# Kernel optimization log

Hardware: AMD Instinct MI355X
Metric: run time of the kernel (lower is better)

## Reference

```python
import jax, jax.numpy as jnp
import numpy as np

CLIP = 50.0
EPS = 1e-8


def _attn_jacobian_agg(q, k, v, scale):
    """Aggregate attention Jacobian dO/dq summed over queries, plus attention outputs.

    q: (B, Q, d); k, v: (B, S, d).
    Per-query Jacobian: J_q = scale * sum_j p_j v_j (k_j - kbar)^T, kbar = sum_i p_i k_i.
    Returns (agg_jac: (B, d, d), outputs: (B, Q, d)).
    """
    scores = jnp.einsum('bqd,bsd->bqs', q, k) * scale
    p = jax.nn.softmax(scores, axis=-1)
    out = jnp.einsum('bqs,bsd->bqd', p, v)           # attention outputs O
    kbar = jnp.einsum('bqs,bsd->bqd', p, k)          # expected key per query
    # sum_j p_j v_j k_j^T  -> (B, Q, d, d)
    pvk = jnp.einsum('bqs,bsd,bse->bqde', p, v, k)
    jac = scale * (pvk - out[..., :, None] * kbar[..., None, :])
    return jac.sum(axis=1), out


def setup_inputs() -> dict:
    key = jax.random.key(0)
    ks = jax.random.split(key, 5)
    B, Q, S, M, D = 256, 16, 512, 8, 128
    return {
        'queries': jax.random.normal(ks[0], (B, Q, D), dtype=jnp.float32),
        'keys':    jax.random.normal(ks[1], (B, S, D), dtype=jnp.float32),
        'values':  jax.random.normal(ks[2], (B, S, D), dtype=jnp.float32),
        'k_cg':    jax.random.normal(ks[3], (B, M, D), dtype=jnp.float32),
        'v_cg':    jax.random.normal(ks[4], (B, M, D), dtype=jnp.float32),
    }


def reference(queries, keys, values, k_cg, v_cg):
    B, Q, d = queries.shape
    scale = d ** -0.5

    dense_jac, dense_out = _attn_jacobian_agg(queries, keys, values, scale)
    cg_jac, cg_out = _attn_jacobian_agg(queries, k_cg, v_cg, scale)

    # jacobian_clip_value = 50.0 (config default)
    dense_jac = jnp.clip(dense_jac, -CLIP, CLIP)
    cg_jac = jnp.clip(cg_jac, -CLIP, CLIP)

    df = dense_jac.reshape(B, -1)
    cf = cg_jac.reshape(B, -1)
    dn = jnp.linalg.norm(df, axis=-1)
    cn = jnp.linalg.norm(cf, axis=-1)
    cosine_sim = (df * cf).sum(axis=-1) / (dn * cn + EPS)
    force_direction_loss = 1.0 - cosine_sim

    # consistency: per-query output MSE, averaged over queries, scaled by 1/d_head
    out_diff = dense_out - cg_out
    per_query_mse = (out_diff ** 2).sum(axis=-1)          # (B, Q)
    consistency_loss = per_query_mse.sum(axis=-1) / Q / d  # (B,)

    # v4 loss: L = w_dir * L_force_cos + w_cons * L_consistency (defaults 1.0, 1.0)
    total = 1.0 * force_direction_loss + 1.0 * consistency_loss
    return total.mean()  # reduction='mean'
```

## Files before the change

kernel.cpp:

```cpp
#include <hip/hip_runtime.h>
#include <math.h>


namespace {
constexpr int Bn = 256, Qn = 16, Sn = 512, Mn = 8, Dn = 128;
constexpr int NT = 512;
constexpr float SCALE = 0.08838834764831845f;
constexpr float CLIPV = 50.0f;

constexpr int W_OFF_F = 1048576;
constexpr int PCG_OFF_B = 4718592;
constexpr int WC_OFF_F = 1196032;
constexpr int PART_OFF_F = 1198080;

typedef __attribute__((ext_vector_type(8))) short bf16x8;
typedef __attribute__((ext_vector_type(4))) float f32x4;
#define MFMA16(a, b, c) __builtin_amdgcn_mfma_f32_16x16x32_bf16((a), (b), (c), 0, 0, 0)

__device__ inline unsigned int pack2t(float a, float b) {
  return __builtin_amdgcn_perm(__builtin_bit_cast(unsigned int, b),
                               __builtin_bit_cast(unsigned int, a), 0x07060302u);
}
__device__ inline unsigned short f2bf(float x) {
  unsigned int u = __builtin_bit_cast(unsigned int, x);
  u += 0x7fffu + ((u >> 16) & 1u);
  return (unsigned short)(u >> 16);
}
__device__ inline float bf2f(unsigned short h) {
  unsigned int u = ((unsigned int)h) << 16;
  return __builtin_bit_cast(float, u);
}
union Frag {
  bf16x8 v;
  unsigned int u[4];
  unsigned short h[8];
};

constexpr int A_QS = 0, A_PB = 4352, A_RDM = 20992, A_RDS = 21504,
              A_CGS = 22016, A_CGP = 22528, A_LDSZ = 22784;

__global__ __launch_bounds__(NT) void scores_kernel(
    const float* __restrict__ Qg, const float* __restrict__ Kg,
    const float* __restrict__ Kcg, float* __restrict__ ws) {
  __shared__ __align__(16) char L[A_LDSZ];
  const int b = blockIdx.x, t = threadIdx.x;
  const int lane = t & 63, wv = t >> 6, quad = lane >> 4, l16 = lane & 15;
  const float* Qb = Qg + (size_t)b * Qn * Dn;
  const float* Kb = Kg + (size_t)b * Sn * Dn;
  const float* Kc = Kcg + (size_t)b * Mn * Dn;

  if (t == 0)
    *(float4*)(ws + PART_OFF_F + b * 4) = make_float4(0.f, 0.f, 0.f, 0.f);

  {
    int row = t >> 5, c4 = t & 31;
    float4 qv = ((const float4*)Qb)[t];
    unsigned int p0 = pack2t(qv.x * SCALE, qv.y * SCALE);
    unsigned int p1 = pack2t(qv.z * SCALE, qv.w * SCALE);
    *(unsigned long long*)(L + A_QS + row * 272 + c4 * 8) =
        (unsigned long long)p0 | ((unsigned long long)p1 << 32);
  }
  __syncthreads();

  bf16x8 aq[4];
#pragma unroll
  for (int kk = 0; kk < 4; ++kk)
    aq[kk] = *(const bf16x8*)(L + A_QS + l16 * 272 + kk * 64 + quad * 16);
  f32x4 acc[4];
#pragma unroll
  for (int j = 0; j < 4; ++j) {
    const float* kp = Kb + (size_t)(64 * wv + 16 * j + l16) * Dn + quad * 8;
    f32x4 a = {0.f, 0.f, 0.f, 0.f};
#pragma unroll
    for (int kk = 0; kk < 4; ++kk) {
      float4 lo = *(const float4*)(kp + kk * 32);
      float4 hi = *(const float4*)(kp + kk * 32 + 4);
      Frag f;
      f.u[0] = pack2t(lo.x, lo.y);
      f.u[1] = pack2t(lo.z, lo.w);
      f.u[2] = pack2t(hi.x, hi.y);
      f.u[3] = pack2t(hi.z, hi.w);
      a = MFMA16(aq[kk], f.v, a);
    }
    acc[j] = a;
  }
  {
    float pm[4];
#pragma unroll
    for (int r = 0; r < 4; ++r)
      pm[r] = fmaxf(fmaxf(acc[0][r], acc[1][r]), fmaxf(acc[2][r], acc[3][r]));
#pragma unroll
    for (int o = 1; o < 16; o <<= 1)
#pragma unroll
      for (int r = 0; r < 4; ++r) pm[r] = fmaxf(pm[r], __shfl_xor(pm[r], o));
    if (l16 == 0)
#pragma unroll
      for (int r = 0; r < 4; ++r) *(float*)(L + A_RDM + (quad * 4 + r) * 32 + wv * 4) = pm[r];
  }
  __syncthreads();
  float gm[4];
#pragma unroll
  for (int r = 0; r < 4; ++r) {
    const float* p = (const float*)(L + A_RDM + (quad * 4 + r) * 32);
    float m = p[0];
#pragma unroll
    for (int w = 1; w < 8; ++w) m = fmaxf(m, p[w]);
    gm[r] = m;
  }
  float e[4][4];
  {
    float ps[4] = {0.f, 0.f, 0.f, 0.f};
#pragma unroll
    for (int j = 0; j < 4; ++j)
#pragma unroll
      for (int r = 0; r < 4; ++r) {
        e[j][r] = __expf(acc[j][r] - gm[r]);
        ps[r] += e[j][r];
      }
#pragma unroll
    for (int o = 1; o < 16; o <<= 1)
#pragma unroll
      for (int r = 0; r < 4; ++r) ps[r] += __shfl_xor(ps[r], o);
    if (l16 == 0)
#pragma unroll
      for (int r = 0; r < 4; ++r) *(float*)(L + A_RDS + (quad * 4 + r) * 32 + wv * 4) = ps[r];
  }
  __syncthreads();
  float inv[4];
#pragma unroll
  for (int r = 0; r < 4; ++r) {
    const float* p = (const float*)(L + A_RDS + (quad * 4 + r) * 32);
    float s = 0.f;
#pragma unroll
    for (int w = 0; w < 8; ++w) s += p[w];
    inv[r] = 1.f / s;
  }
#pragma unroll
  for (int j = 0; j < 4; ++j)
#pragma unroll
    for (int r = 0; r < 4; ++r)
      *(unsigned short*)(L + A_PB + (quad * 4 + r) * 1040 + (64 * wv + 16 * j + l16) * 2) =
          f2bf(e[j][r] * inv[r]);
  __syncthreads();
  {
    float wsum = 0.f;
#pragma unroll
    for (int q = 0; q < Qn; ++q)
      wsum += bf2f(*(const unsigned short*)(L + A_PB + q * 1040 + t * 2));
    ws[W_OFF_F + b * 512 + t] = wsum;
  }
#pragma unroll
  for (int i = 0; i < 2; ++i) {
    int idx = t + i * 512, q = idx >> 6, c = idx & 63;
    *(uint4*)((char*)ws + (size_t)b * 16384 + q * 1024 + c * 16) =
        *(const uint4*)(L + A_PB + q * 1040 + c * 16);
  }
  if (wv == 0) {
    const float* kp = Kc + (size_t)(l16 & 7) * Dn + quad * 8;
    f32x4 a = {0.f, 0.f, 0.f, 0.f};
#pragma unroll
    for (int kk = 0; kk < 4; ++kk) {
      float4 lo = *(const float4*)(kp + kk * 32);
      float4 hi = *(const float4*)(kp + kk * 32 + 4);
      Frag f;
      f.u[0] = pack2t(lo.x, lo.y);
      f.u[1] = pack2t(lo.z, lo.w);
      f.u[2] = pack2t(hi.x, hi.y);
      f.u[3] = pack2t(hi.z, hi.w);
      a = MFMA16(aq[kk], f.v, a);
    }
    if (l16 < 8)
#pragma unroll
      for (int r = 0; r < 4; ++r)
        *(float*)(L + A_CGS + (quad * 4 + r) * 32 + l16 * 4) = a[r];
  }
  __syncthreads();
  if (t < 16) {
    float xs[8];
    float m = -1e30f;
#pragma unroll
    for (int s = 0; s < 8; ++s) {
      xs[s] = *(const float*)(L + A_CGS + t * 32 + s * 4);
      m = fmaxf(m, xs[s]);
    }
    float ssum = 0.f;
#pragma unroll
    for (int s = 0; s < 8; ++s) {
      xs[s] = __expf(xs[s] - m);
      ssum += xs[s];
    }
    float iv = 1.f / ssum;
    uint4 pk = make_uint4(pack2t(xs[0] * iv, xs[1] * iv), pack2t(xs[2] * iv, xs[3] * iv),
                          pack2t(xs[4] * iv, xs[5] * iv), pack2t(xs[6] * iv, xs[7] * iv));
    *(uint4*)(L + A_CGP + t * 16) = pk;
    *(uint4*)((char*)ws + PCG_OFF_B + b * 256 + t * 16) = pk;
  }
  __syncthreads();
  if (t < 8) {
    float s = 0.f;
#pragma unroll
    for (int q = 0; q < Qn; ++q)
      s += bf2f(*(const unsigned short*)(L + A_CGP + q * 16 + t * 2));
    ws[WC_OFF_F + b * 8 + t] = s;
  }
}

constexpr int B_PB = 0, B_WOFF = 16640, B_KT = 18688, B_VT = 37120, B_VTW = 46336,
              B_PCG = 55552, B_WC = 56832, B_RED = 56864, B_LDSZ = 56992;

__global__ __launch_bounds__(NT, 4) void jac_kernel(
    const float* __restrict__ Kg, const float* __restrict__ Vg,
    const float* __restrict__ Kcg, const float* __restrict__ Vcg,
    float* __restrict__ ws) {
  __shared__ __align__(16) char L[B_LDSZ];
  const int g = blockIdx.x;
  const int h = (g >> 3) & 1;
  const int b = (g & 7) | ((g >> 4) << 3);
  const int t = threadIdx.x, lane = t & 63, wv = t >> 6;
  const int quad = lane >> 4, l16 = lane & 15;

  const float* Kb = Kg + (size_t)b * Sn * Dn;
  const float* Vb = Vg + (size_t)b * Sn * Dn;
  const float* Kc = Kcg + (size_t)b * Mn * Dn;
  const float* Vc = Vcg + (size_t)b * Mn * Dn;

  const int dK = t & 127, gK = t >> 7;
  const int dV = t & 63, gV = t >> 6;
  float kpf[2][8], vpf[8];

  auto load_tiles = [&](int st) {
#pragma unroll
    for (int o = 0; o < 2; ++o) {
      int s0 = st * 64 + (gK + 4 * o) * 8;
#pragma unroll
      for (int i = 0; i < 8; ++i) kpf[o][i] = Kb[(size_t)(s0 + i) * Dn + dK];
    }
    int s1 = st * 64 + gV * 8;
#pragma unroll
    for (int i = 0; i < 8; ++i) vpf[i] = Vb[(size_t)(s1 + i) * Dn + h * 64 + dV];
  };
  auto store_tiles = [&](int st) {
#pragma unroll
    for (int o = 0; o < 2; ++o) {
      unsigned int u0 = pack2t(kpf[o][0], kpf[o][1]), u1 = pack2t(kpf[o][2], kpf[o][3]);
      unsigned int u2 = pack2t(kpf[o][4], kpf[o][5]), u3 = pack2t(kpf[o][6], kpf[o][7]);
      *(uint4*)(L + B_KT + dK * 144 + (gK + 4 * o) * 16) = make_uint4(u0, u1, u2, u3);
    }
    int s1 = st * 64 + gV * 8;
    float w8[8];
#pragma unroll
    for (int i = 0; i < 8; ++i) w8[i] = *(const float*)(L + B_WOFF + (s1 + i) * 4);
    *(uint4*)(L + B_VT + dV * 144 + gV * 16) =
        make_uint4(pack2t(vpf[0], vpf[1]), pack2t(vpf[2], vpf[3]),
                   pack2t(vpf[4], vpf[5]), pack2t(vpf[6], vpf[7]));
    *(uint4*)(L + B_VTW + dV * 144 + gV * 16) =
        make_uint4(pack2t(w8[0] * vpf[0], w8[1] * vpf[1]), pack2t(w8[2] * vpf[2], w8[3] * vpf[3]),
                   pack2t(w8[4] * vpf[4], w8[5] * vpf[5]), pack2t(w8[6] * vpf[6], w8[7] * vpf[7]));
  };

#pragma unroll
  for (int i = 0; i < 2; ++i) {
    int idx = t + i * 512, q = idx >> 6, c = idx & 63;
    *(uint4*)(L + B_PB + q * 1040 + c * 16) =
        *(const uint4*)((const char*)ws + (size_t)b * 16384 + q * 1024 + c * 16);
  }
  *(float*)(L + B_WOFF + t * 4) = ws[W_OFF_F + b * 512 + t];
  if (t < 16) {
    uint4 pv = *(const uint4*)((const char*)ws + PCG_OFF_B + b * 256 + t * 16);
    *(uint4*)(L + B_PCG + t * 80) = pv;
    *(uint4*)(L + B_PCG + t * 80 + 16) = make_uint4(0, 0, 0, 0);
    *(uint4*)(L + B_PCG + t * 80 + 32) = make_uint4(0, 0, 0, 0);
    *(uint4*)(L + B_PCG + t * 80 + 48) = make_uint4(0, 0, 0, 0);
  }
  if (t < 8) *(float*)(L + B_WC + t * 4) = ws[WC_OFF_F + b * 8 + t];
  load_tiles(0);
  __syncthreads();

  const int rp = wv & 1, ch = wv >> 1;
  f32x4 C00 = {0.f,0.f,0.f,0.f}, C01 = {0.f,0.f,0.f,0.f};
  f32x4 C10 = {0.f,0.f,0.f,0.f}, C11 = {0.f,0.f,0.f,0.f};
  f32x4 outacc = {0.f,0.f,0.f,0.f}, kbacc = {0.f,0.f,0.f,0.f};

  auto ckstep = [&](int colByte, f32x4& c00, f32x4& c01, f32x4& c10, f32x4& c11) {
    bf16x8 A0 = *(const bf16x8*)(L + B_VTW + (rp * 32 + l16) * 144 + colByte + quad * 16);
    bf16x8 A1 = *(const bf16x8*)(L + B_VTW + (rp * 32 + 16 + l16) * 144 + colByte + quad * 16);
    bf16x8 B0 = *(const bf16x8*)(L + B_KT + (ch * 32 + l16) * 144 + colByte + quad * 16);
    bf16x8 B1 = *(const bf16x8*)(L + B_KT + (ch * 32 + 16 + l16) * 144 + colByte + quad * 16);
    c00 = MFMA16(A0, B0, c00);
    c01 = MFMA16(A0, B1, c01);
    c10 = MFMA16(A1, B0, c10);
    c11 = MFMA16(A1, B1, c11);
  };

  for (int st = 0; st < 8; ++st) {
    if (st) __syncthreads();
    store_tiles(st);
    __syncthreads();
    if (st < 7) load_tiles(st + 1);
#pragma unroll
    for (int z = 0; z < 2; ++z) {
      int colByte = z * 64;
      bf16x8 pA = *(const bf16x8*)(L + B_PB + l16 * 1040 + st * 128 + z * 64 + quad * 16);
      bf16x8 bK = *(const bf16x8*)(L + B_KT + (wv * 16 + l16) * 144 + colByte + quad * 16);
      kbacc = MFMA16(pA, bK, kbacc);
      if (wv < 4) {
        bf16x8 bV = *(const bf16x8*)(L + B_VT + (wv * 16 + l16) * 144 + colByte + quad * 16);
        outacc = MFMA16(pA, bV, outacc);
      }
      ckstep(colByte, C00, C01, C10, C11);
    }
  }
  __syncthreads();

  if (wv < 4) {
#pragma unroll
    for (int r = 0; r < 4; ++r)
      *(unsigned short*)(L + B_VTW + (wv * 16 + l16) * 144 + (quad * 4 + r) * 2) = f2bf(-outacc[r]);
  }
#pragma unroll
  for (int r = 0; r < 4; ++r)
    *(unsigned short*)(L + B_KT + (wv * 16 + l16) * 144 + (quad * 4 + r) * 2) = f2bf(kbacc[r]);
  if (t < 256) {
    *(uint4*)(L + B_KT + (t >> 1) * 144 + 32 + (t & 1) * 16) = make_uint4(0, 0, 0, 0);
  } else if (t < 384) {
    int i = t - 256;
    *(uint4*)(L + B_VTW + (i >> 1) * 144 + 32 + (i & 1) * 16) = make_uint4(0, 0, 0, 0);
  }
  __syncthreads();
  ckstep(0, C00, C01, C10, C11);
#pragma unroll
  for (int r = 0; r < 4; ++r) {
    C00[r] = fminf(fmaxf(SCALE * C00[r], -CLIPV), CLIPV);
    C01[r] = fminf(fmaxf(SCALE * C01[r], -CLIPV), CLIPV);
    C10[r] = fminf(fmaxf(SCALE * C10[r], -CLIPV), CLIPV);
    C11[r] = fminf(fmaxf(SCALE * C11[r], -CLIPV), CLIPV);
  }
  __syncthreads();

  if (t < 128) {
    float kv[8];
#pragma unroll
    for (int i = 0; i < 8; ++i) kv[i] = Kc[(size_t)i * Dn + t];
    *(uint4*)(L + B_KT + t * 144) = make_uint4(pack2t(kv[0], kv[1]), pack2t(kv[2], kv[3]),
                                               pack2t(kv[4], kv[5]), pack2t(kv[6], kv[7]));
    *(uint4*)(L + B_KT + t * 144 + 16) = make_uint4(0, 0, 0, 0);
    *(uint4*)(L + B_KT + t * 144 + 32) = make_uint4(0, 0, 0, 0);
    *(uint4*)(L + B_KT + t * 144 + 48) = make_uint4(0, 0, 0, 0);
  } else if (t < 192) {
    int d = t - 128;
    float v2[8];
#pragma unroll
    for (int i = 0; i < 8; ++i) v2[i] = Vc[(size_t)i * Dn + h * 64 + d];
    *(uint4*)(L + B_VT + d * 144) = make_uint4(pack2t(v2[0], v2[1]), pack2t(v2[2], v2[3]),
                                               pack2t(v2[4], v2[5]), pack2t(v2[6], v2[7]));
    *(uint4*)(L + B_VT + d * 144 + 16) = make_uint4(0, 0, 0, 0);
    *(uint4*)(L + B_VT + d * 144 + 32) = make_uint4(0, 0, 0, 0);
    *(uint4*)(L + B_VT + d * 144 + 48) = make_uint4(0, 0, 0, 0);
  } else if (t < 256) {
    int d = t - 192;
    float v2[8], wc[8];
#pragma unroll
    for (int i = 0; i < 8; ++i) {
      v2[i] = Vc[(size_t)i * Dn + h * 64 + d];
      wc[i] = *(const float*)(L + B_WC + i * 4);
    }
    *(uint4*)(L + B_VTW + d * 144) =
        make_uint4(pack2t(wc[0] * v2[0], wc[1] * v2[1]), pack2t(wc[2] * v2[2], wc[3] * v2[3]),
                   pack2t(wc[4] * v2[4], wc[5] * v2[5]), pack2t(wc[6] * v2[6], wc[7] * v2[7]));
    *(uint4*)(L + B_VTW + d * 144 + 16) = make_uint4(0, 0, 0, 0);
    *(uint4*)(L + B_VTW + d * 144 + 32) = make_uint4(0, 0, 0, 0);
    *(uint4*)(L + B_VTW + d * 144 + 48) = make_uint4(0, 0, 0, 0);
  }
  __syncthreads();
  f32x4 outc = {0.f,0.f,0.f,0.f}, kbc = {0.f,0.f,0.f,0.f};
  f32x4 D00 = {0.f,0.f,0.f,0.f}, D01 = {0.f,0.f,0.f,0.f};
  f32x4 D10 = {0.f,0.f,0.f,0.f}, D11 = {0.f,0.f,0.f,0.f};
  {
    bf16x8 pA = *(const bf16x8*)(L + B_PCG + l16 * 80 + quad * 16);
    bf16x8 bK = *(const bf16x8*)(L + B_KT + (wv * 16 + l16) * 144 + quad * 16);
    kbc = MFMA16(pA, bK, kbc);
    if (wv < 4) {
      bf16x8 bV = *(const bf16x8*)(L + B_VT + (wv * 16 + l16) * 144 + quad * 16);
      outc = MFMA16(pA, bV, outc);
    }
    ckstep(0, D00, D01, D10, D11);
  }
  __syncthreads();
  if (wv < 4) {
#pragma unroll
    for (int r = 0; r < 4; ++r)
      *(unsigned short*)(L + B_VTW + (wv * 16 + l16) * 144 + (quad * 4 + r) * 2) = f2bf(-outc[r]);
  }
#pragma unroll
  for (int r = 0; r < 4; ++r)
    *(unsigned short*)(L + B_KT + (wv * 16 + l16) * 144 + (quad * 4 + r) * 2) = f2bf(kbc[r]);
  __syncthreads();
  ckstep(0, D00, D01, D10, D11);
#pragma unroll
  for (int r = 0; r < 4; ++r) {
    D00[r] = fminf(fmaxf(SCALE * D00[r], -CLIPV), CLIPV);
    D01[r] = fminf(fmaxf(SCALE * D01[r], -CLIPV), CLIPV);
    D10[r] = fminf(fmaxf(SCALE * D10[r], -CLIPV), CLIPV);
    D11[r] = fminf(fmaxf(SCALE * D11[r], -CLIPV), CLIPV);
  }

  float dot = 0.f, nd2 = 0.f, nc2 = 0.f, cons = 0.f;
#pragma unroll
  for (int r = 0; r < 4; ++r) {
    dot += C00[r] * D00[r] + C01[r] * D01[r] + C10[r] * D10[r] + C11[r] * D11[r];
    nd2 += C00[r] * C00[r] + C01[r] * C01[r] + C10[r] * C10[r] + C11[r] * C11[r];
    nc2 += D00[r] * D00[r] + D01[r] * D01[r] + D10[r] * D10[r] + D11[r] * D11[r];
  }
  if (wv < 4) {
#pragma unroll
    for (int r = 0; r < 4; ++r) {
      float df = outacc[r] - outc[r];
      cons += df * df;
    }
  }
#pragma unroll
  for (int o = 32; o; o >>= 1) {
    dot += __shfl_xor(dot, o);
    nd2 += __shfl_xor(nd2, o);
    nc2 += __shfl_xor(nc2, o);
    cons += __shfl_xor(cons, o);
  }
  if (lane == 0) {
    float* red = (float*)(L + B_RED);
    red[wv * 4 + 0] = dot;
    red[wv * 4 + 1] = nd2;
    red[wv * 4 + 2] = nc2;
    red[wv * 4 + 3] = cons;
  }
  __syncthreads();
  if (t == 0) {
    const float* red = (const float*)(L + B_RED);
    float d_ = 0.f, n1 = 0.f, n2 = 0.f, cs = 0.f;
#pragma unroll
    for (int w = 0; w < 8; ++w) {
      d_ += red[w * 4 + 0];
      n1 += red[w * 4 + 1];
      n2 += red[w * 4 + 2];
      cs += red[w * 4 + 3];
    }
    atomicAdd(ws + PART_OFF_F + b * 4 + 0, d_);
    atomicAdd(ws + PART_OFF_F + b * 4 + 1, n1);
    atomicAdd(ws + PART_OFF_F + b * 4 + 2, n2);
    atomicAdd(ws + PART_OFF_F + b * 4 + 3, cs);
  }
}

__global__ void finalize_kernel(const float* __restrict__ ws, float* __restrict__ out) {
  __shared__ float sr[256];
  int i = threadIdx.x;
  const float* p = ws + PART_OFF_F + i * 4;
  float cosv = p[0] / (sqrtf(p[1]) * sqrtf(p[2]) + 1e-8f);
  sr[i] = (1.0f - cosv) + p[3] * (1.0f / (float)(Qn * Dn));
  __syncthreads();
  for (int off = 128; off; off >>= 1) {
    if (i < off) sr[i] += sr[i + off];
    __syncthreads();
  }
  if (i == 0) out[0] = sr[0] * (1.0f / (float)Bn);
}
}

extern "C" void kernel_launch(void* const* d_in, const int* in_sizes, int n_in,
                              void* d_out, int out_size, void* d_ws, size_t ws_size,
                              hipStream_t stream) {
  const float* q = (const float*)d_in[0];
  const float* k = (const float*)d_in[1];
  const float* v = (const float*)d_in[2];
  const float* kc = (const float*)d_in[3];
  const float* vc = (const float*)d_in[4];
  float* out = (float*)d_out;
  float* ws = (float*)d_ws;
  scores_kernel<<<Bn, NT, 0, stream>>>(q, k, kc, ws);
  jac_kernel<<<2 * Bn, NT, 0, stream>>>(k, v, kc, vc, ws);
  finalize_kernel<<<1, 256, 0, stream>>>(ws, out);
}
```

Measured before the change: 171.7 us.

## Split jacobian kernel into four quadrant blocks per batch with staggered tile order

The jacobian kernel now launches four blocks per batch instead of two. Each block computes a 64x64 quadrant of the d×d Jacobian, with K restricted to its half of the columns. The LDS footprint is roughly halved by reading the probability fragments directly from global memory instead of staging them, and launch bounds raise the occupancy target to 8 blocks. A per-quadrant stagger of the S-tile order spreads concurrent reads across blocks. In exchange, each block redundantly recomputes kbar or the outputs for its half, and the four blocks of a batch re-read the K and V columns from global memory.

After: 183.4 us. 1.07x slower.

```diff
diff --git a/kernel.cpp b/kernel.cpp
--- a/kernel.cpp
+++ b/kernel.cpp
@@ -20,6 +20,10 @@
 __device__ inline unsigned int pack2t(float a, float b) {
   return __builtin_amdgcn_perm(__builtin_bit_cast(unsigned int, b),
                                __builtin_bit_cast(unsigned int, a), 0x07060302u);
+}
+__device__ inline uint4 pack8(const float* x) {
+  return make_uint4(pack2t(x[0], x[1]), pack2t(x[2], x[3]),
+                    pack2t(x[4], x[5]), pack2t(x[6], x[7]));
 }
 __device__ inline unsigned short f2bf(float x) {
   unsigned int u = __builtin_bit_cast(unsigned int, x);
@@ -205,17 +209,19 @@
   }
 }
 
-constexpr int B_PB = 0, B_WOFF = 16640, B_KT = 18688, B_VT = 37120, B_VTW = 46336,
-              B_PCG = 55552, B_WC = 56832, B_RED = 56864, B_LDSZ = 56992;
-
-__global__ __launch_bounds__(NT, 4) void jac_kernel(
+constexpr int B_KT = 0, B_VT = 9216, B_VTW = 18432, B_W = 27648,
+              B_PCG = 29696, B_WC = 30976, B_RED = 31008, B_LDSZ = 31136;
+
+__global__ __launch_bounds__(NT, 8) void jac_kernel(
     const float* __restrict__ Kg, const float* __restrict__ Vg,
     const float* __restrict__ Kcg, const float* __restrict__ Vcg,
     float* __restrict__ ws) {
   __shared__ __align__(16) char L[B_LDSZ];
   const int g = blockIdx.x;
-  const int h = (g >> 3) & 1;
-  const int b = (g & 7) | ((g >> 4) << 3);
+  const int b = (g & 7) | ((g >> 5) << 3);
+  const int r4 = (g >> 3) & 3;
+  const int h = r4 >> 1, e2 = r4 & 1;
+  const int stag = r4 * 2;
   const int t = threadIdx.x, lane = t & 63, wv = t >> 6;
   const int quad = lane >> 4, l16 = lane & 15;
 
@@ -223,198 +229,176 @@
   const float* Vb = Vg + (size_t)b * Sn * Dn;
   const float* Kc = Kcg + (size_t)b * Mn * Dn;
   const float* Vc = Vcg + (size_t)b * Mn * Dn;
-
-  const int dK = t & 127, gK = t >> 7;
-  const int dV = t & 63, gV = t >> 6;
-  float kpf[2][8], vpf[8];
-
+  float* Wl = (float*)(L + B_W);
+
+  const int dL = t & 63, oc = t >> 6;
+  const float* Kcol = Kb + e2 * 64 + dL;
+  const float* Vcol = Vb + h * 64 + dL;
+  float kpf[8], vpf[8];
   auto load_tiles = [&](int st) {
-#pragma unroll
-    for (int o = 0; o < 2; ++o) {
-      int s0 = st * 64 + (gK + 4 * o) * 8;
-#pragma unroll
-      for (int i = 0; i < 8; ++i) kpf[o][i] = Kb[(size_t)(s0 + i) * Dn + dK];
-    }
-    int s1 = st * 64 + gV * 8;
-#pragma unroll
-    for (int i = 0; i < 8; ++i) vpf[i] = Vb[(size_t)(s1 + i) * Dn + h * 64 + dV];
+    int s0 = st * 64 + oc * 8;
+#pragma unroll
+    for (int i = 0; i < 8; ++i) {
+      kpf[i] = Kcol[(size_t)(s0 + i) * Dn];
+      vpf[i] = Vcol[(size_t)(s0 + i) * Dn];
+    }
   };
   auto store_tiles = [&](int st) {
-#pragma unroll
-    for (int o = 0; o < 2; ++o) {
-      unsigned int u0 = pack2t(kpf[o][0], kpf[o][1]), u1 = pack2t(kpf[o][2], kpf[o][3]);
-      unsigned int u2 = pack2t(kpf[o][4], kpf[o][5]), u3 = pack2t(kpf[o][6], kpf[o][7]);
-      *(uint4*)(L + B_KT + dK * 144 + (gK + 4 * o) * 16) = make_uint4(u0, u1, u2, u3);
-    }
-    int s1 = st * 64 + gV * 8;
-    float w8[8];
-#pragma unroll
-    for (int i = 0; i < 8; ++i) w8[i] = *(const float*)(L + B_WOFF + (s1 + i) * 4);
-    *(uint4*)(L + B_VT + dV * 144 + gV * 16) =
-        make_uint4(pack2t(vpf[0], vpf[1]), pack2t(vpf[2], vpf[3]),
-                   pack2t(vpf[4], vpf[5]), pack2t(vpf[6], vpf[7]));
-    *(uint4*)(L + B_VTW + dV * 144 + gV * 16) =
-        make_uint4(pack2t(w8[0] * vpf[0], w8[1] * vpf[1]), pack2t(w8[2] * vpf[2], w8[3] * vpf[3]),
-                   pack2t(w8[4] * vpf[4], w8[5] * vpf[5]), pack2t(w8[6] * vpf[6], w8[7] * vpf[7]));
+    int s0 = st * 64 + oc * 8;
+    *(uint4*)(L + B_KT + dL * 144 + oc * 16) = pack8(kpf);
+    *(uint4*)(L + B_VT + dL * 144 + oc * 16) = pack8(vpf);
+    float wvp[8];
+#pragma unroll
+    for (int i = 0; i < 8; ++i) wvp[i] = Wl[s0 + i] * vpf[i];
+    *(uint4*)(L + B_VTW + dL * 144 + oc * 16) = pack8(wvp);
   };
 
-#pragma unroll
-  for (int i = 0; i < 2; ++i) {
-    int idx = t + i * 512, q = idx >> 6, c = idx & 63;
-    *(uint4*)(L + B_PB + q * 1040 + c * 16) =
-        *(const uint4*)((const char*)ws + (size_t)b * 16384 + q * 1024 + c * 16);
-  }
-  *(float*)(L + B_WOFF + t * 4) = ws[W_OFF_F + b * 512 + t];
+  Wl[t] = ws[W_OFF_F + b * 512 + t];
   if (t < 16) {
-    uint4 pv = *(const uint4*)((const char*)ws + PCG_OFF_B + b * 256 + t * 16);
-    *(uint4*)(L + B_PCG + t * 80) = pv;
+    *(uint4*)(L + B_PCG + t * 80) = *(const uint4*)((const char*)ws + PCG_OFF_B + b * 256 + t * 16);
     *(uint4*)(L + B_PCG + t * 80 + 16) = make_uint4(0, 0, 0, 0);
     *(uint4*)(L + B_PCG + t * 80 + 32) = make_uint4(0, 0, 0, 0);
     *(uint4*)(L + B_PCG + t * 80 + 48) = make_uint4(0, 0, 0, 0);
   }
   if (t < 8) *(float*)(L + B_WC + t * 4) = ws[WC_OFF_F + b * 8 + t];
-  load_tiles(0);
-  __syncthreads();
-
-  const int rp = wv & 1, ch = wv >> 1;
-  f32x4 C00 = {0.f,0.f,0.f,0.f}, C01 = {0.f,0.f,0.f,0.f};
-  f32x4 C10 = {0.f,0.f,0.f,0.f}, C11 = {0.f,0.f,0.f,0.f};
-  f32x4 outacc = {0.f,0.f,0.f,0.f}, kbacc = {0.f,0.f,0.f,0.f};
-
-  auto ckstep = [&](int colByte, f32x4& c00, f32x4& c01, f32x4& c10, f32x4& c11) {
-    bf16x8 A0 = *(const bf16x8*)(L + B_VTW + (rp * 32 + l16) * 144 + colByte + quad * 16);
-    bf16x8 A1 = *(const bf16x8*)(L + B_VTW + (rp * 32 + 16 + l16) * 144 + colByte + quad * 16);
-    bf16x8 B0 = *(const bf16x8*)(L + B_KT + (ch * 32 + l16) * 144 + colByte + quad * 16);
-    bf16x8 B1 = *(const bf16x8*)(L + B_KT + (ch * 32 + 16 + l16) * 144 + colByte + quad * 16);
-    c00 = MFMA16(A0, B0, c00);
-    c01 = MFMA16(A0, B1, c01);
-    c10 = MFMA16(A1, B0, c10);
-    c11 = MFMA16(A1, B1, c11);
-  };
-
-  for (int st = 0; st < 8; ++st) {
-    if (st) __syncthreads();
+  load_tiles(stag);
+  __syncthreads();
+
+  const int rp = wv & 3, ch = wv >> 2;
+  const int auxRow = (wv & 3) * 16 + l16;
+  const char* auxBase = L + (wv < 4 ? B_KT : B_VT) + auxRow * 144;
+  f32x4 Ca = {0.f, 0.f, 0.f, 0.f}, Cb = {0.f, 0.f, 0.f, 0.f}, aux = {0.f, 0.f, 0.f, 0.f};
+  const char* Arow = L + B_VTW + (rp * 16 + l16) * 144;
+  const char* Brow0 = L + B_KT + (ch * 32 + l16) * 144;
+  const char* Brow1 = Brow0 + 16 * 144;
+  const char* Pbase = (const char*)ws + (size_t)b * 16384 + l16 * 1024 + quad * 16;
+
+  for (int it = 0; it < 8; ++it) {
+    int st = (it + stag) & 7;
+    if (it) __syncthreads();
     store_tiles(st);
     __syncthreads();
-    if (st < 7) load_tiles(st + 1);
+    if (it < 7) load_tiles((it + 1 + stag) & 7);
+    bf16x8 p0 = *(const bf16x8*)(Pbase + st * 128);
+    bf16x8 p1 = *(const bf16x8*)(Pbase + st * 128 + 64);
 #pragma unroll
     for (int z = 0; z < 2; ++z) {
-      int colByte = z * 64;
-      bf16x8 pA = *(const bf16x8*)(L + B_PB + l16 * 1040 + st * 128 + z * 64 + quad * 16);
-      bf16x8 bK = *(const bf16x8*)(L + B_KT + (wv * 16 + l16) * 144 + colByte + quad * 16);
-      kbacc = MFMA16(pA, bK, kbacc);
-      if (wv < 4) {
-        bf16x8 bV = *(const bf16x8*)(L + B_VT + (wv * 16 + l16) * 144 + colByte + quad * 16);
-        outacc = MFMA16(pA, bV, outacc);
-      }
-      ckstep(colByte, C00, C01, C10, C11);
-    }
-  }
-  __syncthreads();
-
-  if (wv < 4) {
+      int cB = z * 64 + quad * 16;
+      bf16x8 fx = *(const bf16x8*)(auxBase + cB);
+      aux = MFMA16(z ? p1 : p0, fx, aux);
+      bf16x8 A0 = *(const bf16x8*)(Arow + cB);
+      bf16x8 B0 = *(const bf16x8*)(Brow0 + cB);
+      bf16x8 B1 = *(const bf16x8*)(Brow1 + cB);
+      Ca = MFMA16(A0, B0, Ca);
+      Cb = MFMA16(A0, B1, Cb);
+    }
+  }
+  __syncthreads();
+
+  {
+    char* tgt = (char*)(L + (wv < 4 ? B_KT : B_VTW) + auxRow * 144);
+    float sgn = (wv < 4) ? 1.f : -1.f;
 #pragma unroll
     for (int r = 0; r < 4; ++r)
-      *(unsigned short*)(L + B_VTW + (wv * 16 + l16) * 144 + (quad * 4 + r) * 2) = f2bf(-outacc[r]);
-  }
-#pragma unroll
-  for (int r = 0; r < 4; ++r)
-    *(unsigned short*)(L + B_KT + (wv * 16 + l16) * 144 + (quad * 4 + r) * 2) = f2bf(kbacc[r]);
-  if (t < 256) {
+      *(unsigned short*)(tgt + (quad * 4 + r) * 2) = f2bf(sgn * aux[r]);
+  }
+  if (t < 128) {
     *(uint4*)(L + B_KT + (t >> 1) * 144 + 32 + (t & 1) * 16) = make_uint4(0, 0, 0, 0);
-  } else if (t < 384) {
-    int i = t - 256;
+  } else if (t < 256) {
+    int i = t - 128;
     *(uint4*)(L + B_VTW + (i >> 1) * 144 + 32 + (i & 1) * 16) = make_uint4(0, 0, 0, 0);
   }
   __syncthreads();
-  ckstep(0, C00, C01, C10, C11);
+  {
+    int cB = quad * 16;
+    bf16x8 A0 = *(const bf16x8*)(Arow + cB);
+    bf16x8 B0 = *(const bf16x8*)(Brow0 + cB);
+    bf16x8 B1 = *(const bf16x8*)(Brow1 + cB);
+    Ca = MFMA16(A0, B0, Ca);
+    Cb = MFMA16(A0, B1, Cb);
+  }
 #pragma unroll
   for (int r = 0; r < 4; ++r) {
-    C00[r] = fminf(fmaxf(SCALE * C00[r], -CLIPV), CLIPV);
-    C01[r] = fminf(fmaxf(SCALE * C01[r], -CLIPV), CLIPV);
-    C10[r] = fminf(fmaxf(SCALE * C10[r], -CLIPV), CLIPV);
-    C11[r] = fminf(fmaxf(SCALE * C11[r], -CLIPV), CLIPV);
-  }
-  __syncthreads();
-
-  if (t < 128) {
+    Ca[r] = fminf(fmaxf(SCALE * Ca[r], -CLIPV), CLIPV);
+    Cb[r] = fminf(fmaxf(SCALE * Cb[r], -CLIPV), CLIPV);
+  }
+  __syncthreads();
+
+  if (t < 64) {
     float kv[8];
 #pragma unroll
-    for (int i = 0; i < 8; ++i) kv[i] = Kc[(size_t)i * Dn + t];
-    *(uint4*)(L + B_KT + t * 144) = make_uint4(pack2t(kv[0], kv[1]), pack2t(kv[2], kv[3]),
-                                               pack2t(kv[4], kv[5]), pack2t(kv[6], kv[7]));
+    for (int i = 0; i < 8; ++i) kv[i] = Kc[(size_t)i * Dn + e2 * 64 + t];
+    *(uint4*)(L + B_KT + t * 144) = pack8(kv);
     *(uint4*)(L + B_KT + t * 144 + 16) = make_uint4(0, 0, 0, 0);
     *(uint4*)(L + B_KT + t * 144 + 32) = make_uint4(0, 0, 0, 0);
     *(uint4*)(L + B_KT + t * 144 + 48) = make_uint4(0, 0, 0, 0);
-  } else if (t < 192) {
-    int d = t - 128;
+  } else if (t < 128) {
+    int d = t - 64;
     float v2[8];
 #pragma unroll
     for (int i = 0; i < 8; ++i) v2[i] = Vc[(size_t)i * Dn + h * 64 + d];
-    *(uint4*)(L + B_VT + d * 144) = make_uint4(pack2t(v2[0], v2[1]), pack2t(v2[2], v2[3]),
-                                               pack2t(v2[4], v2[5]), pack2t(v2[6], v2[7]));
+    *(uint4*)(L + B_VT + d * 144) = pack8(v2);
     *(uint4*)(L + B_VT + d * 144 + 16) = make_uint4(0, 0, 0, 0);
     *(uint4*)(L + B_VT + d * 144 + 32) = make_uint4(0, 0, 0, 0);
     *(uint4*)(L + B_VT + d * 144 + 48) = make_uint4(0, 0, 0, 0);
-  } else if (t < 256) {
-    int d = t - 192;
-    float v2[8], wc[8];
-#pragma unroll
-    for (int i = 0; i < 8; ++i) {
-      v2[i] = Vc[(size_t)i * Dn + h * 64 + d];
-      wc[i] = *(const float*)(L + B_WC + i * 4);
-    }
-    *(uint4*)(L + B_VTW + d * 144) =
-        make_uint4(pack2t(wc[0] * v2[0], wc[1] * v2[1]), pack2t(wc[2] * v2[2], wc[3] * v2[3]),
-                   pack2t(wc[4] * v2[4], wc[5] * v2[5]), pack2t(wc[6] * v2[6], wc[7] * v2[7]));
+  } else if (t < 192) {
+    int d = t - 128;
+    float wvp[8];
+#pragma unroll
+    for (int i = 0; i < 8; ++i)
+      wvp[i] = Vc[(size_t)i * Dn + h * 64 + d] * *(const float*)(L + B_WC + i * 4);
+    *(uint4*)(L + B_VTW + d * 144) = pack8(wvp);
     *(uint4*)(L + B_VTW + d * 144 + 16) = make_uint4(0, 0, 0, 0);
     *(uint4*)(L + B_VTW + d * 144 + 32) = make_uint4(0, 0, 0, 0);
     *(uint4*)(L + B_VTW + d * 144 + 48) = make_uint4(0, 0, 0, 0);
   }
   __syncthreads();
-  f32x4 outc = {0.f,0.f,0.f,0.f}, kbc = {0.f,0.f,0.f,0.f};
-  f32x4 D00 = {0.f,0.f,0.f,0.f}, D01 = {0.f,0.f,0.f,0.f};
-  f32x4 D10 = {0.f,0.f,0.f,0.f}, D11 = {0.f,0.f,0.f,0.f};
-  {
-    bf16x8 pA = *(const bf16x8*)(L + B_PCG + l16 * 80 + quad * 16);
-    bf16x8 bK = *(const bf16x8*)(L + B_KT + (wv * 16 + l16) * 144 + quad * 16);
-    kbc = MFMA16(pA, bK, kbc);
-    if (wv < 4) {
-      bf16x8 bV = *(const bf16x8*)(L + B_VT + (wv * 16 + l16) * 144 + quad * 16);
-      outc = MFMA16(pA, bV, outc);
-    }
-    ckstep(0, D00, D01, D10, D11);
-  }
-  __syncthreads();
-  if (wv < 4) {
+  f32x4 Da = {0.f, 0.f, 0.f, 0.f}, Db = {0.f, 0.f, 0.f, 0.f}, auxc = {0.f, 0.f, 0.f, 0.f};
+  {
+    int cB = quad * 16;
+    bf16x8 pc = *(const bf16x8*)(L + B_PCG + l16 * 80 + cB);
+    bf16x8 fx = *(const bf16x8*)(auxBase + cB);
+    auxc = MFMA16(pc, fx, auxc);
+    bf16x8 A0 = *(const bf16x8*)(Arow + cB);
+    bf16x8 B0 = *(const bf16x8*)(Brow0 + cB);
+    bf16x8 B1 = *(const bf16x8*)(Brow1 + cB);
+    Da = MFMA16(A0, B0, Da);
+    Db = MFMA16(A0, B1, Db);
+  }
+  __syncthreads();
+  {
+    char* tgt = (char*)(L + (wv < 4 ? B_KT : B_VTW) + auxRow * 144);
+    float sgn = (wv < 4) ? 1.f : -1.f;
 #pragma unroll
     for (int r = 0; r < 4; ++r)
-      *(unsigned short*)(L + B_VTW + (wv * 16 + l16) * 144 + (quad * 4 + r) * 2) = f2bf(-outc[r]);
-  }
-#pragma unroll
-  for (int r = 0; r < 4; ++r)
-    *(unsigned short*)(L + B_KT + (wv * 16 + l16) * 144 + (quad * 4 + r) * 2) = f2bf(kbc[r]);
-  __syncthreads();
-  ckstep(0, D00, D01, D10, D11);
+      *(unsigned short*)(tgt + (quad * 4 + r) * 2) = f2bf(sgn * auxc[r]);
+  }
+  __syncthreads();
+  {
+    int cB = quad * 16;
+    bf16x8 A0 = *(const bf16x8*)(Arow + cB);
+    bf16x8 B0 = *(const bf16x8*)(Brow0 + cB);
+    bf16x8 B1 = *(const bf16x8*)(Brow1 + cB);
+    Da = MFMA16(A0, B0, Da);
+    Db = MFMA16(A0, B1, Db);
+  }
 #pragma unroll
   for (int r = 0; r < 4; ++r) {
-    D00[r] = fminf(fmaxf(SCALE * D00[r], -CLIPV), CLIPV);
-    D01[r] = fminf(fmaxf(SCALE * D01[r], -CLIPV), CLIPV);
-    D10[r] = fminf(fmaxf(SCALE * D10[r], -CLIPV), CLIPV);
-    D11[r] = fminf(fmaxf(SCALE * D11[r], -CLIPV), CLIPV);
+    Da[r] = fminf(fmaxf(SCALE * Da[r], -CLIPV), CLIPV);
+    Db[r] = fminf(fmaxf(SCALE * Db[r], -CLIPV), CLIPV);
   }
 
   float dot = 0.f, nd2 = 0.f, nc2 = 0.f, cons = 0.f;
 #pragma unroll
   for (int r = 0; r < 4; ++r) {
-    dot += C00[r] * D00[r] + C01[r] * D01[r] + C10[r] * D10[r] + C11[r] * D11[r];
-    nd2 += C00[r] * C00[r] + C01[r] * C01[r] + C10[r] * C10[r] + C11[r] * C11[r];
-    nc2 += D00[r] * D00[r] + D01[r] * D01[r] + D10[r] * D10[r] + D11[r] * D11[r];
-  }
-  if (wv < 4) {
+    dot += Ca[r] * Da[r] + Cb[r] * Db[r];
+    nd2 += Ca[r] * Ca[r] + Cb[r] * Cb[r];
+    nc2 += Da[r] * Da[r] + Db[r] * Db[r];
+  }
+  if (wv >= 4 && e2 == 0) {
 #pragma unroll
     for (int r = 0; r < 4; ++r) {
-      float df = outacc[r] - outc[r];
+      float df = aux[r] - auxc[r];
       cons += df * df;
     }
   }
@@ -476,6 +460,6 @@
   float* out = (float*)d_out;
   float* ws = (float*)d_ws;
   scores_kernel<<<Bn, NT, 0, stream>>>(q, k, kc, ws);
-  jac_kernel<<<2 * Bn, NT, 0, stream>>>(k, v, kc, vc, ws);
+  jac_kernel<<<4 * Bn, NT, 0, stream>>>(k, v, kc, vc, ws);
   finalize_kernel<<<1, 256, 0, stream>>>(ws, out);
 }
```
